# Optimization experiments

Measured on AMD Instinct MI355X. Metric: run time of the kernel, lower is better.

## Reference

```python
import jax, jax.numpy as jnp
import numpy as np

N_HEADS, D_MODEL, D_HEAD = 16, 1024, 64
BATCH, SEQ = 2, 2048
INIT_RANGE = 0.02


def setup_inputs() -> dict:
    key = jax.random.key(0)
    ks = jax.random.split(key, 5)
    x = jax.random.normal(ks[0], (BATCH, SEQ, D_MODEL), dtype=jnp.float32)
    W_Q = jax.random.normal(ks[1], (N_HEADS, D_MODEL, D_HEAD), dtype=jnp.float32) * INIT_RANGE
    W_K = jax.random.normal(ks[2], (N_HEADS, D_MODEL, D_HEAD), dtype=jnp.float32) * INIT_RANGE
    W_V = jax.random.normal(ks[3], (N_HEADS, D_MODEL, D_HEAD), dtype=jnp.float32) * INIT_RANGE
    W_O = jax.random.normal(ks[4], (N_HEADS, D_HEAD, D_MODEL), dtype=jnp.float32) * INIT_RANGE
    b_Q = jnp.zeros((N_HEADS, D_HEAD), dtype=jnp.float32)
    b_K = jnp.zeros((N_HEADS, D_HEAD), dtype=jnp.float32)
    b_V = jnp.zeros((N_HEADS, D_HEAD), dtype=jnp.float32)
    b_O = jnp.zeros((D_MODEL,), dtype=jnp.float32)
    return {"normalized_resid_pre": x, "W_Q": W_Q, "W_K": W_K, "W_V": W_V,
            "W_O": W_O, "b_Q": b_Q, "b_K": b_K, "b_V": b_V, "b_O": b_O}


def reference(normalized_resid_pre, W_Q, W_K, W_V, W_O, b_Q, b_K, b_V, b_O):
    x = normalized_resid_pre  # [b, s, d_model]
    q = jnp.einsum('bsm,hmd->bshd', x, W_Q) + b_Q  # [b, s, h, d_head]
    k = jnp.einsum('bsm,hmd->bshd', x, W_K) + b_K
    v = jnp.einsum('bsm,hmd->bshd', x, W_V) + b_V
    scores = jnp.einsum('bqhd,bkhd->bhqk', q, k) / jnp.sqrt(jnp.float32(D_HEAD))
    seq = x.shape[1]
    causal = jnp.tril(jnp.ones((seq, seq), dtype=bool))  # True where allowed
    scores = jnp.where(causal, scores, jnp.float32(-jnp.inf))
    pattern = jax.nn.softmax(scores, axis=-1)  # [b, h, q, k]
    z = jnp.einsum('bhqk,bkhd->bqhd', pattern, v)
    attn_out = jnp.einsum('bqhd,hdm->bqm', z, W_O) + b_O
    return attn_out
```

## Files before the change

kernel.cpp:

```cpp
#include <hip/hip_runtime.h>
#include <hip/hip_bf16.h>

#define BATCH 2
#define SEQL 2048
#define NH 16
#define DH 64
#define DM 1024
#define LDK 72
#define QSCALE 0.1803368801111244f
#define NTASKS 1024u

typedef __hip_bfloat16 bf16;
typedef __attribute__((ext_vector_type(8))) short  bf16x8;
typedef __attribute__((ext_vector_type(4))) float  f32x4;

__device__ __forceinline__ void gl_lds16(const void* g, void* l) {
    __builtin_amdgcn_global_load_lds(
        (const __attribute__((address_space(1))) unsigned int*)g,
        (__attribute__((address_space(3))) unsigned int*)l, 16, 0, 0);
}

__global__ __launch_bounds__(256) void xconv_kernel(
    const float* __restrict__ x, bf16* __restrict__ xb)
{
    const size_t i = ((size_t)blockIdx.x * 256 + threadIdx.x) * 4;
    const float4 v = *(const float4*)(x + i);
    bf16 o[4];
    o[0] = __float2bfloat16(v.x); o[1] = __float2bfloat16(v.y);
    o[2] = __float2bfloat16(v.z); o[3] = __float2bfloat16(v.w);
    *(uint2*)(xb + i) = *(const uint2*)o;
}

__global__ __launch_bounds__(256) void wtrans_kernel(
    const float* __restrict__ Wq, const float* __restrict__ Wk,
    const float* __restrict__ Wv, const float* __restrict__ Wo,
    bf16* __restrict__ Wt)
{
    __shared__ float ts[64][65];
    const int zi = blockIdx.z;
    const float* src = (zi == 0) ? Wq : (zi == 1) ? Wk : (zi == 2) ? Wv : Wo;
    bf16* dst = Wt + (size_t)zi * DM * DM;
    const int row0 = blockIdx.y * 64;
    const int col0 = blockIdx.x * 64;
    const int tx = threadIdx.x & 63;
    const int ty = threadIdx.x >> 6;

    if (zi < 3) {
        const int h = col0 >> 6;
        #pragma unroll
        for (int i = 0; i < 16; ++i) {
            const int r = ty + 4 * i;
            ts[r][tx] = src[h * (DM * DH) + (row0 + r) * DH + tx];
        }
    } else {
        #pragma unroll
        for (int i = 0; i < 16; ++i) {
            const int r = ty + 4 * i;
            ts[r][tx] = src[(size_t)(row0 + r) * DM + col0 + tx];
        }
    }
    __syncthreads();
    #pragma unroll
    for (int i = 0; i < 16; ++i) {
        const int rr = ty + 4 * i;
        dst[(size_t)(col0 + rr) * DM + row0 + tx] = __float2bfloat16(ts[tx][rr]);
    }
}

__global__ __launch_bounds__(256) void qkv_gemm(
    const bf16* __restrict__ xb, const bf16* __restrict__ Wt,
    const float* __restrict__ bq, const float* __restrict__ bk, const float* __restrict__ bv,
    bf16* __restrict__ qkv)
{
    __shared__ __align__(16) bf16 As[128 * 32];
    __shared__ __align__(16) bf16 Bs[128 * 32];

    const int t = threadIdx.x;
    const int lane = t & 63, w = t >> 6;
    const int ml = lane & 15, quad = lane >> 4;
    const int wr = w >> 1, wc = w & 1;
    const int bn = blockIdx.x, bm = blockIdx.y, which = blockIdx.z;

    const bf16* A0 = xb + (size_t)(bm * 128) * DM;
    const bf16* B0 = Wt + (size_t)which * DM * DM + (size_t)(bn * 128) * DM;
    const float* bias = (which == 0) ? bq : (which == 1) ? bk : bv;
    bf16* outb = qkv + (size_t)which * (BATCH * SEQL * NH * DH);
    const float oscale = (which == 0) ? QSCALE : 1.0f;

    f32x4 acc[4][4];
    #pragma unroll
    for (int i = 0; i < 4; ++i)
        #pragma unroll
        for (int j = 0; j < 4; ++j) acc[i][j] = (f32x4){0.f, 0.f, 0.f, 0.f};

    for (int kt = 0; kt < DM / 32; ++kt) {
        const int k0 = kt * 32;
        __syncthreads();
        #pragma unroll
        for (int j = 0; j < 2; ++j) {
            const int flat = t + j * 256;
            const int r = flat >> 2, c = (flat & 3) * 8;
            gl_lds16(A0 + (size_t)r * DM + k0 + c, &As[flat * 8]);
            gl_lds16(B0 + (size_t)r * DM + k0 + c, &Bs[flat * 8]);
        }
        __syncthreads();
        bf16x8 af[4], bfr[4];
        #pragma unroll
        for (int i = 0; i < 4; ++i)
            af[i] = *(const bf16x8*)&As[(wr * 64 + i * 16 + ml) * 32 + quad * 8];
        #pragma unroll
        for (int j = 0; j < 4; ++j)
            bfr[j] = *(const bf16x8*)&Bs[(wc * 64 + j * 16 + ml) * 32 + quad * 8];
        #pragma unroll
        for (int i = 0; i < 4; ++i)
            #pragma unroll
            for (int j = 0; j < 4; ++j)
                acc[i][j] = __builtin_amdgcn_mfma_f32_16x16x32_bf16(af[i], bfr[j], acc[i][j], 0, 0, 0);
    }

    float bb[4];
    #pragma unroll
    for (int j = 0; j < 4; ++j) bb[j] = bias[bn * 128 + wc * 64 + j * 16 + ml];

    if (which == 2) {
        #pragma unroll
        for (int i = 0; i < 4; ++i) {
            const int row0v = bm * 128 + wr * 64 + i * 16 + quad * 4;
            const int b = row0v >> 11;
            const int s0 = row0v & (SEQL - 1);
            #pragma unroll
            for (int j = 0; j < 4; ++j) {
                const int col = bn * 128 + wc * 64 + j * 16 + ml;
                const int h = col >> 6, d = col & 63;
                bf16 tmp[4];
                #pragma unroll
                for (int rg = 0; rg < 4; ++rg)
                    tmp[rg] = __float2bfloat16(acc[i][j][rg] + bb[j]);
                *(uint2*)&outb[(((size_t)(b * NH + h)) * DH + d) * SEQL + s0] =
                    *(const uint2*)tmp;
            }
        }
    } else {
        #pragma unroll
        for (int i = 0; i < 4; ++i) {
            #pragma unroll
            for (int rg = 0; rg < 4; ++rg) {
                const int row = bm * 128 + wr * 64 + i * 16 + quad * 4 + rg;
                const int b = row >> 11;
                const int s = row & (SEQL - 1);
                #pragma unroll
                for (int j = 0; j < 4; ++j) {
                    const int col = bn * 128 + wc * 64 + j * 16 + ml;
                    const int h = col >> 6, d = col & 63;
                    outb[(((size_t)(b * NH + h)) * SEQL + s) * DH + d] =
                        __float2bfloat16((acc[i][j][rg] + bb[j]) * oscale);
                }
            }
        }
    }
}

__global__ __launch_bounds__(256) void oproj_gemm(
    const bf16* __restrict__ zb, const bf16* __restrict__ Bt,
    const float* __restrict__ bo, float* __restrict__ out)
{
    __shared__ __align__(16) bf16 As[128 * 32];
    __shared__ __align__(16) bf16 Bs[64 * 32];

    const int t = threadIdx.x;
    const int lane = t & 63, w = t >> 6;
    const int ml = lane & 15, quad = lane >> 4;
    const int wr = w >> 1, wc = w & 1;
    const int bn = blockIdx.x, bm = blockIdx.y;

    const bf16* A0 = zb + (size_t)(bm * 128) * DM;
    const bf16* B0 = Bt + (size_t)(bn * 64) * DM;

    f32x4 acc[4][2];
    #pragma unroll
    for (int i = 0; i < 4; ++i)
        #pragma unroll
        for (int j = 0; j < 2; ++j) acc[i][j] = (f32x4){0.f, 0.f, 0.f, 0.f};

    for (int kt = 0; kt < DM / 32; ++kt) {
        const int k0 = kt * 32;
        __syncthreads();
        {
            const int r0 = t >> 2, c0 = (t & 3) * 8;
            gl_lds16(A0 + (size_t)r0 * DM + k0 + c0, &As[t * 8]);
            const int f1 = t + 256;
            const int r1 = f1 >> 2, c1 = (f1 & 3) * 8;
            gl_lds16(A0 + (size_t)r1 * DM + k0 + c1, &As[f1 * 8]);
            gl_lds16(B0 + (size_t)r0 * DM + k0 + c0, &Bs[t * 8]);
        }
        __syncthreads();
        bf16x8 af[4], bfr[2];
        #pragma unroll
        for (int i = 0; i < 4; ++i)
            af[i] = *(const bf16x8*)&As[(wr * 64 + i * 16 + ml) * 32 + quad * 8];
        #pragma unroll
        for (int j = 0; j < 2; ++j)
            bfr[j] = *(const bf16x8*)&Bs[(wc * 32 + j * 16 + ml) * 32 + quad * 8];
        #pragma unroll
        for (int i = 0; i < 4; ++i)
            #pragma unroll
            for (int j = 0; j < 2; ++j)
                acc[i][j] = __builtin_amdgcn_mfma_f32_16x16x32_bf16(af[i], bfr[j], acc[i][j], 0, 0, 0);
    }

    float bb[2];
    #pragma unroll
    for (int j = 0; j < 2; ++j) bb[j] = bo[bn * 64 + wc * 32 + j * 16 + ml];

    #pragma unroll
    for (int i = 0; i < 4; ++i) {
        #pragma unroll
        for (int rg = 0; rg < 4; ++rg) {
            const int row = bm * 128 + wr * 64 + i * 16 + quad * 4 + rg;
            #pragma unroll
            for (int j = 0; j < 2; ++j) {
                const int col = bn * 64 + wc * 32 + j * 16 + ml;
                out[(size_t)row * DM + col] = acc[i][j][rg] + bb[j];
            }
        }
    }
}

__global__ __launch_bounds__(256) void attn_kernel(
    const bf16* __restrict__ qg, const bf16* __restrict__ kg, const bf16* __restrict__ vtg,
    bf16* __restrict__ z, unsigned* __restrict__ counter)
{
    __shared__ bf16 KsS[64 * LDK];
    __shared__ bf16 VtS[64 * LDK];
    __shared__ bf16 PsS[4][16 * LDK];
    __shared__ unsigned taskS;

    const int t    = threadIdx.x;
    const int lane = t & 63;
    const int w    = t >> 6;
    const int m    = lane & 15;
    const int quad = lane >> 4;

    const int rp = t >> 3;
    const int d0 = (t & 7) * 8;

    const short ob = (m == 0) ? (short)0x3F80 : (short)0;
    const bf16x8 bones = {ob, ob, ob, ob, ob, ob, ob, ob};

    bf16* Psw = PsS[w];

    for (;;) {
        __syncthreads();
        if (t == 0) taskS = atomicAdd(counter, 1u);
        __syncthreads();
        const unsigned task = taskS;
        if (task >= NTASKS) break;

        const int qt = 31 - (int)(task >> 5);
        const int bh = (int)(task & 31u);
        const int b  = bh >> 4;
        const int h  = bh & 15;
        const int q0 = qt * 64;

        const size_t base   = (size_t)bh * SEQL * DH;
        const size_t vtbase = (size_t)bh * DH * SEQL;

        bf16x8 aq[2];
        {
            const bf16* qp = qg + base + (size_t)(q0 + w * 16 + m) * DH + quad * 8;
            aq[0] = *(const bf16x8*)(qp);
            aq[1] = *(const bf16x8*)(qp + 32);
        }

        f32x4 zacc[4];
        #pragma unroll
        for (int nt = 0; nt < 4; ++nt) zacc[nt] = (f32x4){0.f, 0.f, 0.f, 0.f};
        f32x4 lacc = (f32x4){0.f, 0.f, 0.f, 0.f};

        for (int kt = 0; kt <= qt; ++kt) {
            __syncthreads();
            {
                const bf16* kr = kg + base + (size_t)(kt * 64 + 2 * rp) * DH + d0;
                const bf16* vr = vtg + vtbase + (size_t)(2 * rp) * SEQL + kt * 64 + d0;
                const uint4 k0 = *(const uint4*)(kr);
                const uint4 k1 = *(const uint4*)(kr + DH);
                const uint4 v0 = *(const uint4*)(vr);
                const uint4 v1 = *(const uint4*)(vr + SEQL);
                *(uint4*)(&KsS[(2 * rp) * LDK + d0])     = k0;
                *(uint4*)(&KsS[(2 * rp + 1) * LDK + d0]) = k1;
                *(uint4*)(&VtS[(2 * rp) * LDK + d0])     = v0;
                *(uint4*)(&VtS[(2 * rp + 1) * LDK + d0]) = v1;
            }
            __syncthreads();

            f32x4 sc[4];
            #pragma unroll
            for (int nt = 0; nt < 4; ++nt) sc[nt] = (f32x4){0.f, 0.f, 0.f, 0.f};
            #pragma unroll
            for (int ks = 0; ks < 2; ++ks) {
                #pragma unroll
                for (int nt = 0; nt < 4; ++nt) {
                    const bf16x8 bk = *(const bf16x8*)(&KsS[(nt * 16 + m) * LDK + ks * 32 + quad * 8]);
                    sc[nt] = __builtin_amdgcn_mfma_f32_16x16x32_bf16(aq[ks], bk, sc[nt], 0, 0, 0);
                }
            }
            if (kt == qt) {
                #pragma unroll
                for (int nt = 0; nt < 4; ++nt) {
                    const int col = nt * 16 + m;
                    #pragma unroll
                    for (int rg = 0; rg < 4; ++rg) {
                        const int row = w * 16 + quad * 4 + rg;
                        if (col > row) sc[nt][rg] = -1e30f;
                    }
                }
            }

            #pragma unroll
            for (int nt = 0; nt < 4; ++nt)
                #pragma unroll
                for (int rg = 0; rg < 4; ++rg)
                    Psw[(quad * 4 + rg) * LDK + nt * 16 + m] =
                        __float2bfloat16(__builtin_exp2f(sc[nt][rg]));

            #pragma unroll
            for (int ks = 0; ks < 2; ++ks) {
                const bf16x8 ap = *(const bf16x8*)(&Psw[m * LDK + ks * 32 + quad * 8]);
                lacc = __builtin_amdgcn_mfma_f32_16x16x32_bf16(ap, bones, lacc, 0, 0, 0);
                #pragma unroll
                for (int nt = 0; nt < 4; ++nt) {
                    const bf16x8 bv = *(const bf16x8*)(&VtS[(nt * 16 + m) * LDK + ks * 32 + quad * 8]);
                    zacc[nt] = __builtin_amdgcn_mfma_f32_16x16x32_bf16(ap, bv, zacc[nt], 0, 0, 0);
                }
            }
        }

        float invl[4];
        #pragma unroll
        for (int rg = 0; rg < 4; ++rg)
            invl[rg] = 1.f / __shfl(lacc[rg], quad * 16);
        #pragma unroll
        for (int nt = 0; nt < 4; ++nt) {
            const int d = nt * 16 + m;
            #pragma unroll
            for (int rg = 0; rg < 4; ++rg) {
                const int qrow = q0 + w * 16 + quad * 4 + rg;
                z[(((size_t)b * SEQL + qrow) * NH + h) * DH + d] =
                    __float2bfloat16(zacc[nt][rg] * invl[rg]);
            }
        }
    }
}

extern "C" void kernel_launch(void* const* d_in, const int* in_sizes, int n_in,
                              void* d_out, int out_size, void* d_ws, size_t ws_size,
                              hipStream_t stream)
{
    const float* x  = (const float*)d_in[0];
    const float* Wq = (const float*)d_in[1];
    const float* Wk = (const float*)d_in[2];
    const float* Wv = (const float*)d_in[3];
    const float* Wo = (const float*)d_in[4];
    const float* bq = (const float*)d_in[5];
    const float* bk = (const float*)d_in[6];
    const float* bv = (const float*)d_in[7];
    const float* bo = (const float*)d_in[8];
    float* out = (float*)d_out;

    const size_t TOK = (size_t)BATCH * SEQL;
    const size_t QKV = TOK * DM;
    bf16* xb  = (bf16*)d_ws;
    bf16* Wt  = xb + QKV;
    bf16* qkv = Wt + 4 * (size_t)DM * DM;
    bf16* zb  = qkv + 3 * QKV;
    unsigned* counter = (unsigned*)(zb + QKV);

    hipMemsetAsync(counter, 0, sizeof(unsigned), stream);
    xconv_kernel<<<dim3(TOK * DM / 1024), 256, 0, stream>>>(x, xb);
    wtrans_kernel<<<dim3(16, 16, 4), 256, 0, stream>>>(Wq, Wk, Wv, Wo, Wt);
    qkv_gemm<<<dim3(8, 32, 3), 256, 0, stream>>>(xb, Wt, bq, bk, bv, qkv);
    attn_kernel<<<dim3(512), 256, 0, stream>>>(
        qkv, qkv + QKV, qkv + 2 * QKV, zb, counter);
    oproj_gemm<<<dim3(16, 32), 256, 0, stream>>>(zb, Wt + 3 * (size_t)DM * DM, bo, out);
}
```

Baseline: 205.5 us.

## Replace atomic persistent attention scheduler with static grid; vectorize Q/K epilogue stores

The attention kernel no longer runs as a persistent kernel that pulls tasks from an atomic counter. It now launches one block per (batch*head, query tile), with the largest query tiles given the lowest blockIdx.y, which removes the counter memset, the atomics and the per-task barriers. The QKV GEMM swaps the A and B fragment sources for the Q and K outputs so each lane holds four consecutive head dimensions, allowing packed 8-byte stores and a float4 bias load instead of scalar stores. The risk is that the static grid depends on the hardware dispatcher for load balance across uneven causal tiles.

```diff
diff --git a/kernel.cpp b/kernel.cpp
--- a/kernel.cpp
+++ b/kernel.cpp
@@ -8,7 +8,6 @@
 #define DM 1024
 #define LDK 72
 #define QSCALE 0.1803368801111244f
-#define NTASKS 1024u
 
 typedef __hip_bfloat16 bf16;
 typedef __attribute__((ext_vector_type(8))) short  bf16x8;
@@ -87,6 +86,9 @@
     bf16* outb = qkv + (size_t)which * (BATCH * SEQL * NH * DH);
     const float oscale = (which == 0) ? QSCALE : 1.0f;
 
+    const bf16* AfragSrc = (which == 2) ? As : Bs;
+    const bf16* BfragSrc = (which == 2) ? Bs : As;
+
     f32x4 acc[4][4];
     #pragma unroll
     for (int i = 0; i < 4; ++i)
@@ -107,10 +109,10 @@
         bf16x8 af[4], bfr[4];
         #pragma unroll
         for (int i = 0; i < 4; ++i)
-            af[i] = *(const bf16x8*)&As[(wr * 64 + i * 16 + ml) * 32 + quad * 8];
+            af[i] = *(const bf16x8*)&AfragSrc[(wr * 64 + i * 16 + ml) * 32 + quad * 8];
         #pragma unroll
         for (int j = 0; j < 4; ++j)
-            bfr[j] = *(const bf16x8*)&Bs[(wc * 64 + j * 16 + ml) * 32 + quad * 8];
+            bfr[j] = *(const bf16x8*)&BfragSrc[(wc * 64 + j * 16 + ml) * 32 + quad * 8];
         #pragma unroll
         for (int i = 0; i < 4; ++i)
             #pragma unroll
@@ -118,11 +120,10 @@
                 acc[i][j] = __builtin_amdgcn_mfma_f32_16x16x32_bf16(af[i], bfr[j], acc[i][j], 0, 0, 0);
     }
 
-    float bb[4];
-    #pragma unroll
-    for (int j = 0; j < 4; ++j) bb[j] = bias[bn * 128 + wc * 64 + j * 16 + ml];
-
     if (which == 2) {
+        float bb[4];
+        #pragma unroll
+        for (int j = 0; j < 4; ++j) bb[j] = bias[bn * 128 + wc * 64 + j * 16 + ml];
         #pragma unroll
         for (int i = 0; i < 4; ++i) {
             const int row0v = bm * 128 + wr * 64 + i * 16 + quad * 4;
@@ -143,18 +144,21 @@
     } else {
         #pragma unroll
         for (int i = 0; i < 4; ++i) {
-            #pragma unroll
-            for (int rg = 0; rg < 4; ++rg) {
-                const int row = bm * 128 + wr * 64 + i * 16 + quad * 4 + rg;
-                const int b = row >> 11;
-                const int s = row & (SEQL - 1);
+            const int hd0 = bn * 128 + wr * 64 + i * 16 + quad * 4;
+            const int h = hd0 >> 6, d0 = hd0 & 63;
+            const float4 bb4 = *(const float4*)&bias[hd0];
+            const float bbv[4] = {bb4.x, bb4.y, bb4.z, bb4.w};
+            #pragma unroll
+            for (int j = 0; j < 4; ++j) {
+                const int tok = bm * 128 + wc * 64 + j * 16 + ml;
+                const int b = tok >> 11;
+                const int s = tok & (SEQL - 1);
+                bf16 tmp[4];
                 #pragma unroll
-                for (int j = 0; j < 4; ++j) {
-                    const int col = bn * 128 + wc * 64 + j * 16 + ml;
-                    const int h = col >> 6, d = col & 63;
-                    outb[(((size_t)(b * NH + h)) * SEQL + s) * DH + d] =
-                        __float2bfloat16((acc[i][j][rg] + bb[j]) * oscale);
-                }
+                for (int rg = 0; rg < 4; ++rg)
+                    tmp[rg] = __float2bfloat16((acc[i][j][rg] + bbv[rg]) * oscale);
+                *(uint2*)&outb[(((size_t)(b * NH + h)) * SEQL + s) * DH + d0] =
+                    *(const uint2*)tmp;
             }
         }
     }
@@ -228,12 +232,11 @@
 
 __global__ __launch_bounds__(256) void attn_kernel(
     const bf16* __restrict__ qg, const bf16* __restrict__ kg, const bf16* __restrict__ vtg,
-    bf16* __restrict__ z, unsigned* __restrict__ counter)
+    bf16* __restrict__ z)
 {
     __shared__ bf16 KsS[64 * LDK];
     __shared__ bf16 VtS[64 * LDK];
     __shared__ bf16 PsS[4][16 * LDK];
-    __shared__ unsigned taskS;
 
     const int t    = threadIdx.x;
     const int lane = t & 63;
@@ -241,113 +244,105 @@
     const int m    = lane & 15;
     const int quad = lane >> 4;
 
+    const int bh = blockIdx.x;
+    const int b  = bh >> 4;
+    const int h  = bh & 15;
+    const int qt = (gridDim.y - 1) - blockIdx.y;
+    const int q0 = qt * 64;
+
+    const size_t base   = (size_t)bh * SEQL * DH;
+    const size_t vtbase = (size_t)bh * DH * SEQL;
+
     const int rp = t >> 3;
     const int d0 = (t & 7) * 8;
 
+    bf16x8 aq[2];
+    {
+        const bf16* qp = qg + base + (size_t)(q0 + w * 16 + m) * DH + quad * 8;
+        aq[0] = *(const bf16x8*)(qp);
+        aq[1] = *(const bf16x8*)(qp + 32);
+    }
+
     const short ob = (m == 0) ? (short)0x3F80 : (short)0;
     const bf16x8 bones = {ob, ob, ob, ob, ob, ob, ob, ob};
 
+    f32x4 zacc[4];
+    #pragma unroll
+    for (int nt = 0; nt < 4; ++nt) zacc[nt] = (f32x4){0.f, 0.f, 0.f, 0.f};
+    f32x4 lacc = (f32x4){0.f, 0.f, 0.f, 0.f};
+
     bf16* Psw = PsS[w];
 
-    for (;;) {
-        __syncthreads();
-        if (t == 0) taskS = atomicAdd(counter, 1u);
-        __syncthreads();
-        const unsigned task = taskS;
-        if (task >= NTASKS) break;
-
-        const int qt = 31 - (int)(task >> 5);
-        const int bh = (int)(task & 31u);
-        const int b  = bh >> 4;
-        const int h  = bh & 15;
-        const int q0 = qt * 64;
-
-        const size_t base   = (size_t)bh * SEQL * DH;
-        const size_t vtbase = (size_t)bh * DH * SEQL;
-
-        bf16x8 aq[2];
+    for (int kt = 0; kt <= qt; ++kt) {
+        __syncthreads();
         {
-            const bf16* qp = qg + base + (size_t)(q0 + w * 16 + m) * DH + quad * 8;
-            aq[0] = *(const bf16x8*)(qp);
-            aq[1] = *(const bf16x8*)(qp + 32);
-        }
-
-        f32x4 zacc[4];
-        #pragma unroll
-        for (int nt = 0; nt < 4; ++nt) zacc[nt] = (f32x4){0.f, 0.f, 0.f, 0.f};
-        f32x4 lacc = (f32x4){0.f, 0.f, 0.f, 0.f};
-
-        for (int kt = 0; kt <= qt; ++kt) {
-            __syncthreads();
-            {
-                const bf16* kr = kg + base + (size_t)(kt * 64 + 2 * rp) * DH + d0;
-                const bf16* vr = vtg + vtbase + (size_t)(2 * rp) * SEQL + kt * 64 + d0;
-                const uint4 k0 = *(const uint4*)(kr);
-                const uint4 k1 = *(const uint4*)(kr + DH);
-                const uint4 v0 = *(const uint4*)(vr);
-                const uint4 v1 = *(const uint4*)(vr + SEQL);
-                *(uint4*)(&KsS[(2 * rp) * LDK + d0])     = k0;
-                *(uint4*)(&KsS[(2 * rp + 1) * LDK + d0]) = k1;
-                *(uint4*)(&VtS[(2 * rp) * LDK + d0])     = v0;
-                *(uint4*)(&VtS[(2 * rp + 1) * LDK + d0]) = v1;
-            }
-            __syncthreads();
-
-            f32x4 sc[4];
-            #pragma unroll
-            for (int nt = 0; nt < 4; ++nt) sc[nt] = (f32x4){0.f, 0.f, 0.f, 0.f};
-            #pragma unroll
-            for (int ks = 0; ks < 2; ++ks) {
+            const bf16* kr = kg + base + (size_t)(kt * 64 + 2 * rp) * DH + d0;
+            const bf16* vr = vtg + vtbase + (size_t)(2 * rp) * SEQL + kt * 64 + d0;
+            const uint4 k0 = *(const uint4*)(kr);
+            const uint4 k1 = *(const uint4*)(kr + DH);
+            const uint4 v0 = *(const uint4*)(vr);
+            const uint4 v1 = *(const uint4*)(vr + SEQL);
+            *(uint4*)(&KsS[(2 * rp) * LDK + d0])     = k0;
+            *(uint4*)(&KsS[(2 * rp + 1) * LDK + d0]) = k1;
+            *(uint4*)(&VtS[(2 * rp) * LDK + d0])     = v0;
+            *(uint4*)(&VtS[(2 * rp + 1) * LDK + d0]) = v1;
+        }
+        __syncthreads();
+
+        f32x4 sc[4];
+        #pragma unroll
+        for (int nt = 0; nt < 4; ++nt) sc[nt] = (f32x4){0.f, 0.f, 0.f, 0.f};
+        #pragma unroll
+        for (int ks = 0; ks < 2; ++ks) {
+            #pragma unroll
+            for (int nt = 0; nt < 4; ++nt) {
+                const bf16x8 bk = *(const bf16x8*)(&KsS[(nt * 16 + m) * LDK + ks * 32 + quad * 8]);
+                sc[nt] = __builtin_amdgcn_mfma_f32_16x16x32_bf16(aq[ks], bk, sc[nt], 0, 0, 0);
+            }
+        }
+        if (kt == qt) {
+            #pragma unroll
+            for (int nt = 0; nt < 4; ++nt) {
+                const int col = nt * 16 + m;
                 #pragma unroll
-                for (int nt = 0; nt < 4; ++nt) {
-                    const bf16x8 bk = *(const bf16x8*)(&KsS[(nt * 16 + m) * LDK + ks * 32 + quad * 8]);
-                    sc[nt] = __builtin_amdgcn_mfma_f32_16x16x32_bf16(aq[ks], bk, sc[nt], 0, 0, 0);
+                for (int rg = 0; rg < 4; ++rg) {
+                    const int row = w * 16 + quad * 4 + rg;
+                    if (col > row) sc[nt][rg] = -1e30f;
                 }
             }
-            if (kt == qt) {
-                #pragma unroll
-                for (int nt = 0; nt < 4; ++nt) {
-                    const int col = nt * 16 + m;
-                    #pragma unroll
-                    for (int rg = 0; rg < 4; ++rg) {
-                        const int row = w * 16 + quad * 4 + rg;
-                        if (col > row) sc[nt][rg] = -1e30f;
-                    }
-                }
-            }
-
-            #pragma unroll
-            for (int nt = 0; nt < 4; ++nt)
-                #pragma unroll
-                for (int rg = 0; rg < 4; ++rg)
-                    Psw[(quad * 4 + rg) * LDK + nt * 16 + m] =
-                        __float2bfloat16(__builtin_exp2f(sc[nt][rg]));
-
-            #pragma unroll
-            for (int ks = 0; ks < 2; ++ks) {
-                const bf16x8 ap = *(const bf16x8*)(&Psw[m * LDK + ks * 32 + quad * 8]);
-                lacc = __builtin_amdgcn_mfma_f32_16x16x32_bf16(ap, bones, lacc, 0, 0, 0);
-                #pragma unroll
-                for (int nt = 0; nt < 4; ++nt) {
-                    const bf16x8 bv = *(const bf16x8*)(&VtS[(nt * 16 + m) * LDK + ks * 32 + quad * 8]);
-                    zacc[nt] = __builtin_amdgcn_mfma_f32_16x16x32_bf16(ap, bv, zacc[nt], 0, 0, 0);
-                }
-            }
-        }
-
-        float invl[4];
-        #pragma unroll
-        for (int rg = 0; rg < 4; ++rg)
-            invl[rg] = 1.f / __shfl(lacc[rg], quad * 16);
-        #pragma unroll
-        for (int nt = 0; nt < 4; ++nt) {
-            const int d = nt * 16 + m;
-            #pragma unroll
-            for (int rg = 0; rg < 4; ++rg) {
-                const int qrow = q0 + w * 16 + quad * 4 + rg;
-                z[(((size_t)b * SEQL + qrow) * NH + h) * DH + d] =
-                    __float2bfloat16(zacc[nt][rg] * invl[rg]);
-            }
+        }
+
+        #pragma unroll
+        for (int nt = 0; nt < 4; ++nt)
+            #pragma unroll
+            for (int rg = 0; rg < 4; ++rg)
+                Psw[(quad * 4 + rg) * LDK + nt * 16 + m] =
+                    __float2bfloat16(__builtin_exp2f(sc[nt][rg]));
+
+        #pragma unroll
+        for (int ks = 0; ks < 2; ++ks) {
+            const bf16x8 ap = *(const bf16x8*)(&Psw[m * LDK + ks * 32 + quad * 8]);
+            lacc = __builtin_amdgcn_mfma_f32_16x16x32_bf16(ap, bones, lacc, 0, 0, 0);
+            #pragma unroll
+            for (int nt = 0; nt < 4; ++nt) {
+                const bf16x8 bv = *(const bf16x8*)(&VtS[(nt * 16 + m) * LDK + ks * 32 + quad * 8]);
+                zacc[nt] = __builtin_amdgcn_mfma_f32_16x16x32_bf16(ap, bv, zacc[nt], 0, 0, 0);
+            }
+        }
+    }
+
+    float invl[4];
+    #pragma unroll
+    for (int rg = 0; rg < 4; ++rg)
+        invl[rg] = 1.f / __shfl(lacc[rg], quad * 16);
+    #pragma unroll
+    for (int nt = 0; nt < 4; ++nt) {
+        const int d = nt * 16 + m;
+        #pragma unroll
+        for (int rg = 0; rg < 4; ++rg) {
+            const int qrow = q0 + w * 16 + quad * 4 + rg;
+            z[(((size_t)b * SEQL + qrow) * NH + h) * DH + d] =
+                __float2bfloat16(zacc[nt][rg] * invl[rg]);
         }
     }
 }
@@ -373,13 +368,11 @@
     bf16* Wt  = xb + QKV;
     bf16* qkv = Wt + 4 * (size_t)DM * DM;
     bf16* zb  = qkv + 3 * QKV;
-    unsigned* counter = (unsigned*)(zb + QKV);
-
-    hipMemsetAsync(counter, 0, sizeof(unsigned), stream);
+
     xconv_kernel<<<dim3(TOK * DM / 1024), 256, 0, stream>>>(x, xb);
     wtrans_kernel<<<dim3(16, 16, 4), 256, 0, stream>>>(Wq, Wk, Wv, Wo, Wt);
     qkv_gemm<<<dim3(8, 32, 3), 256, 0, stream>>>(xb, Wt, bq, bk, bv, qkv);
-    attn_kernel<<<dim3(512), 256, 0, stream>>>(
-        qkv, qkv + QKV, qkv + 2 * QKV, zb, counter);
+    attn_kernel<<<dim3(BATCH * NH, SEQL / 64), 256, 0, stream>>>(
+        qkv, qkv + QKV, qkv + 2 * QKV, zb);
     oproj_gemm<<<dim3(16, 32), 256, 0, stream>>>(zb, Wt + 3 * (size_t)DM * DM, bo, out);
 }
```

After: 209.8 us. +2.1%, slower.

## Double K-step per barrier in GEMMs and use static grid for attention

Applied to the files above, without the earlier changes.

The QKV and output-projection GEMMs now load two 32-wide K slices per iteration into doubled LDS buffers. This halves the number of barrier pairs per K loop. The attention kernel drops its persistent atomic work-queue and memset and launches one block per (batch-head, query tile), with the longest tiles issued first by reversing blockIdx.y. This removes atomic and memset overhead but relies on the hardware scheduler for load balance across causal tiles of uneven length.

```diff
diff --git a/kernel.cpp b/kernel.cpp
--- a/kernel.cpp
+++ b/kernel.cpp
@@ -8,7 +8,6 @@
 #define DM 1024
 #define LDK 72
 #define QSCALE 0.1803368801111244f
-#define NTASKS 1024u
 
 typedef __hip_bfloat16 bf16;
 typedef __attribute__((ext_vector_type(8))) short  bf16x8;
@@ -72,8 +71,8 @@
     const float* __restrict__ bq, const float* __restrict__ bk, const float* __restrict__ bv,
     bf16* __restrict__ qkv)
 {
-    __shared__ __align__(16) bf16 As[128 * 32];
-    __shared__ __align__(16) bf16 Bs[128 * 32];
+    __shared__ __align__(16) bf16 As[2][128 * 32];
+    __shared__ __align__(16) bf16 Bs[2][128 * 32];
 
     const int t = threadIdx.x;
     const int lane = t & 63, w = t >> 6;
@@ -93,29 +92,37 @@
         #pragma unroll
         for (int j = 0; j < 4; ++j) acc[i][j] = (f32x4){0.f, 0.f, 0.f, 0.f};
 
-    for (int kt = 0; kt < DM / 32; ++kt) {
-        const int k0 = kt * 32;
-        __syncthreads();
-        #pragma unroll
-        for (int j = 0; j < 2; ++j) {
-            const int flat = t + j * 256;
-            const int r = flat >> 2, c = (flat & 3) * 8;
-            gl_lds16(A0 + (size_t)r * DM + k0 + c, &As[flat * 8]);
-            gl_lds16(B0 + (size_t)r * DM + k0 + c, &Bs[flat * 8]);
-        }
-        __syncthreads();
-        bf16x8 af[4], bfr[4];
-        #pragma unroll
-        for (int i = 0; i < 4; ++i)
-            af[i] = *(const bf16x8*)&As[(wr * 64 + i * 16 + ml) * 32 + quad * 8];
-        #pragma unroll
-        for (int j = 0; j < 4; ++j)
-            bfr[j] = *(const bf16x8*)&Bs[(wc * 64 + j * 16 + ml) * 32 + quad * 8];
-        #pragma unroll
-        for (int i = 0; i < 4; ++i)
+    const int r0 = t >> 2, c0 = (t & 3) * 8;
+    const int f1 = t + 256;
+    const int r1 = f1 >> 2, c1 = (f1 & 3) * 8;
+
+    for (int kt = 0; kt < DM / 64; ++kt) {
+        const int k0 = kt * 64;
+        __syncthreads();
+        #pragma unroll
+        for (int half = 0; half < 2; ++half) {
+            const int kh = k0 + half * 32;
+            gl_lds16(A0 + (size_t)r0 * DM + kh + c0, &As[half][t * 8]);
+            gl_lds16(A0 + (size_t)r1 * DM + kh + c1, &As[half][f1 * 8]);
+            gl_lds16(B0 + (size_t)r0 * DM + kh + c0, &Bs[half][t * 8]);
+            gl_lds16(B0 + (size_t)r1 * DM + kh + c1, &Bs[half][f1 * 8]);
+        }
+        __syncthreads();
+        #pragma unroll
+        for (int half = 0; half < 2; ++half) {
+            bf16x8 af[4], bfr[4];
+            #pragma unroll
+            for (int i = 0; i < 4; ++i)
+                af[i] = *(const bf16x8*)&As[half][(wr * 64 + i * 16 + ml) * 32 + quad * 8];
             #pragma unroll
             for (int j = 0; j < 4; ++j)
-                acc[i][j] = __builtin_amdgcn_mfma_f32_16x16x32_bf16(af[i], bfr[j], acc[i][j], 0, 0, 0);
+                bfr[j] = *(const bf16x8*)&Bs[half][(wc * 64 + j * 16 + ml) * 32 + quad * 8];
+            #pragma unroll
+            for (int i = 0; i < 4; ++i)
+                #pragma unroll
+                for (int j = 0; j < 4; ++j)
+                    acc[i][j] = __builtin_amdgcn_mfma_f32_16x16x32_bf16(af[i], bfr[j], acc[i][j], 0, 0, 0);
+        }
     }
 
     float bb[4];
@@ -164,8 +171,8 @@
     const bf16* __restrict__ zb, const bf16* __restrict__ Bt,
     const float* __restrict__ bo, float* __restrict__ out)
 {
-    __shared__ __align__(16) bf16 As[128 * 32];
-    __shared__ __align__(16) bf16 Bs[64 * 32];
+    __shared__ __align__(16) bf16 As[2][128 * 32];
+    __shared__ __align__(16) bf16 Bs[2][64 * 32];
 
     const int t = threadIdx.x;
     const int lane = t & 63, w = t >> 6;
@@ -182,30 +189,36 @@
         #pragma unroll
         for (int j = 0; j < 2; ++j) acc[i][j] = (f32x4){0.f, 0.f, 0.f, 0.f};
 
-    for (int kt = 0; kt < DM / 32; ++kt) {
-        const int k0 = kt * 32;
-        __syncthreads();
-        {
-            const int r0 = t >> 2, c0 = (t & 3) * 8;
-            gl_lds16(A0 + (size_t)r0 * DM + k0 + c0, &As[t * 8]);
-            const int f1 = t + 256;
-            const int r1 = f1 >> 2, c1 = (f1 & 3) * 8;
-            gl_lds16(A0 + (size_t)r1 * DM + k0 + c1, &As[f1 * 8]);
-            gl_lds16(B0 + (size_t)r0 * DM + k0 + c0, &Bs[t * 8]);
-        }
-        __syncthreads();
-        bf16x8 af[4], bfr[2];
-        #pragma unroll
-        for (int i = 0; i < 4; ++i)
-            af[i] = *(const bf16x8*)&As[(wr * 64 + i * 16 + ml) * 32 + quad * 8];
-        #pragma unroll
-        for (int j = 0; j < 2; ++j)
-            bfr[j] = *(const bf16x8*)&Bs[(wc * 32 + j * 16 + ml) * 32 + quad * 8];
-        #pragma unroll
-        for (int i = 0; i < 4; ++i)
+    const int r0 = t >> 2, c0 = (t & 3) * 8;
+    const int f1 = t + 256;
+    const int r1 = f1 >> 2, c1 = (f1 & 3) * 8;
+
+    for (int kt = 0; kt < DM / 64; ++kt) {
+        const int k0 = kt * 64;
+        __syncthreads();
+        #pragma unroll
+        for (int half = 0; half < 2; ++half) {
+            const int kh = k0 + half * 32;
+            gl_lds16(A0 + (size_t)r0 * DM + kh + c0, &As[half][t * 8]);
+            gl_lds16(A0 + (size_t)r1 * DM + kh + c1, &As[half][f1 * 8]);
+            gl_lds16(B0 + (size_t)r0 * DM + kh + c0, &Bs[half][t * 8]);
+        }
+        __syncthreads();
+        #pragma unroll
+        for (int half = 0; half < 2; ++half) {
+            bf16x8 af[4], bfr[2];
+            #pragma unroll
+            for (int i = 0; i < 4; ++i)
+                af[i] = *(const bf16x8*)&As[half][(wr * 64 + i * 16 + ml) * 32 + quad * 8];
             #pragma unroll
             for (int j = 0; j < 2; ++j)
-                acc[i][j] = __builtin_amdgcn_mfma_f32_16x16x32_bf16(af[i], bfr[j], acc[i][j], 0, 0, 0);
+                bfr[j] = *(const bf16x8*)&Bs[half][(wc * 32 + j * 16 + ml) * 32 + quad * 8];
+            #pragma unroll
+            for (int i = 0; i < 4; ++i)
+                #pragma unroll
+                for (int j = 0; j < 2; ++j)
+                    acc[i][j] = __builtin_amdgcn_mfma_f32_16x16x32_bf16(af[i], bfr[j], acc[i][j], 0, 0, 0);
+        }
     }
 
     float bb[2];
@@ -228,12 +241,11 @@
 
 __global__ __launch_bounds__(256) void attn_kernel(
     const bf16* __restrict__ qg, const bf16* __restrict__ kg, const bf16* __restrict__ vtg,
-    bf16* __restrict__ z, unsigned* __restrict__ counter)
+    bf16* __restrict__ z)
 {
     __shared__ bf16 KsS[64 * LDK];
     __shared__ bf16 VtS[64 * LDK];
     __shared__ bf16 PsS[4][16 * LDK];
-    __shared__ unsigned taskS;
 
     const int t    = threadIdx.x;
     const int lane = t & 63;
@@ -241,113 +253,105 @@
     const int m    = lane & 15;
     const int quad = lane >> 4;
 
+    const int bh = blockIdx.x;
+    const int b  = bh >> 4;
+    const int h  = bh & 15;
+    const int qt = (gridDim.y - 1) - blockIdx.y;
+    const int q0 = qt * 64;
+
+    const size_t base   = (size_t)bh * SEQL * DH;
+    const size_t vtbase = (size_t)bh * DH * SEQL;
+
     const int rp = t >> 3;
     const int d0 = (t & 7) * 8;
 
+    bf16x8 aq[2];
+    {
+        const bf16* qp = qg + base + (size_t)(q0 + w * 16 + m) * DH + quad * 8;
+        aq[0] = *(const bf16x8*)(qp);
+        aq[1] = *(const bf16x8*)(qp + 32);
+    }
+
     const short ob = (m == 0) ? (short)0x3F80 : (short)0;
     const bf16x8 bones = {ob, ob, ob, ob, ob, ob, ob, ob};
 
+    f32x4 zacc[4];
+    #pragma unroll
+    for (int nt = 0; nt < 4; ++nt) zacc[nt] = (f32x4){0.f, 0.f, 0.f, 0.f};
+    f32x4 lacc = (f32x4){0.f, 0.f, 0.f, 0.f};
+
     bf16* Psw = PsS[w];
 
-    for (;;) {
-        __syncthreads();
-        if (t == 0) taskS = atomicAdd(counter, 1u);
-        __syncthreads();
-        const unsigned task = taskS;
-        if (task >= NTASKS) break;
-
-        const int qt = 31 - (int)(task >> 5);
-        const int bh = (int)(task & 31u);
-        const int b  = bh >> 4;
-        const int h  = bh & 15;
-        const int q0 = qt * 64;
-
-        const size_t base   = (size_t)bh * SEQL * DH;
-        const size_t vtbase = (size_t)bh * DH * SEQL;
-
-        bf16x8 aq[2];
+    for (int kt = 0; kt <= qt; ++kt) {
+        __syncthreads();
         {
-            const bf16* qp = qg + base + (size_t)(q0 + w * 16 + m) * DH + quad * 8;
-            aq[0] = *(const bf16x8*)(qp);
-            aq[1] = *(const bf16x8*)(qp + 32);
-        }
-
-        f32x4 zacc[4];
-        #pragma unroll
-        for (int nt = 0; nt < 4; ++nt) zacc[nt] = (f32x4){0.f, 0.f, 0.f, 0.f};
-        f32x4 lacc = (f32x4){0.f, 0.f, 0.f, 0.f};
-
-        for (int kt = 0; kt <= qt; ++kt) {
-            __syncthreads();
-            {
-                const bf16* kr = kg + base + (size_t)(kt * 64 + 2 * rp) * DH + d0;
-                const bf16* vr = vtg + vtbase + (size_t)(2 * rp) * SEQL + kt * 64 + d0;
-                const uint4 k0 = *(const uint4*)(kr);
-                const uint4 k1 = *(const uint4*)(kr + DH);
-                const uint4 v0 = *(const uint4*)(vr);
-                const uint4 v1 = *(const uint4*)(vr + SEQL);
-                *(uint4*)(&KsS[(2 * rp) * LDK + d0])     = k0;
-                *(uint4*)(&KsS[(2 * rp + 1) * LDK + d0]) = k1;
-                *(uint4*)(&VtS[(2 * rp) * LDK + d0])     = v0;
-                *(uint4*)(&VtS[(2 * rp + 1) * LDK + d0]) = v1;
-            }
-            __syncthreads();
-
-            f32x4 sc[4];
-            #pragma unroll
-            for (int nt = 0; nt < 4; ++nt) sc[nt] = (f32x4){0.f, 0.f, 0.f, 0.f};
-            #pragma unroll
-            for (int ks = 0; ks < 2; ++ks) {
-                #pragma unroll
-                for (int nt = 0; nt < 4; ++nt) {
-                    const bf16x8 bk = *(const bf16x8*)(&KsS[(nt * 16 + m) * LDK + ks * 32 + quad * 8]);
-                    sc[nt] = __builtin_amdgcn_mfma_f32_16x16x32_bf16(aq[ks], bk, sc[nt], 0, 0, 0);
+            const bf16* kr = kg + base + (size_t)(kt * 64 + 2 * rp) * DH + d0;
+            const bf16* vr = vtg + vtbase + (size_t)(2 * rp) * SEQL + kt * 64 + d0;
+            const uint4 k0 = *(const uint4*)(kr);
+            const uint4 k1 = *(const uint4*)(kr + DH);
+            const uint4 v0 = *(const uint4*)(vr);
+            const uint4 v1 = *(const uint4*)(vr + SEQL);
+            *(uint4*)(&KsS[(2 * rp) * LDK + d0])     = k0;
+            *(uint4*)(&KsS[(2 * rp + 1) * LDK + d0]) = k1;
+            *(uint4*)(&VtS[(2 * rp) * LDK + d0])     = v0;
+            *(uint4*)(&VtS[(2 * rp + 1) * LDK + d0]) = v1;
+        }
+        __syncthreads();
+
+        f32x4 sc[4];
+        #pragma unroll
+        for (int nt = 0; nt < 4; ++nt) sc[nt] = (f32x4){0.f, 0.f, 0.f, 0.f};
+        #pragma unroll
+        for (int ks = 0; ks < 2; ++ks) {
+            #pragma unroll
+            for (int nt = 0; nt < 4; ++nt) {
+                const bf16x8 bk = *(const bf16x8*)(&KsS[(nt * 16 + m) * LDK + ks * 32 + quad * 8]);
+                sc[nt] = __builtin_amdgcn_mfma_f32_16x16x32_bf16(aq[ks], bk, sc[nt], 0, 0, 0);
+            }
+        }
+        if (kt == qt) {
+            #pragma unroll
+            for (int nt = 0; nt < 4; ++nt) {
+                const int col = nt * 16 + m;
+                #pragma unroll
+                for (int rg = 0; rg < 4; ++rg) {
+                    const int row = w * 16 + quad * 4 + rg;
+                    if (col > row) sc[nt][rg] = -1e30f;
                 }
             }
-            if (kt == qt) {
-                #pragma unroll
-                for (int nt = 0; nt < 4; ++nt) {
-                    const int col = nt * 16 + m;
-                    #pragma unroll
-                    for (int rg = 0; rg < 4; ++rg) {
-                        const int row = w * 16 + quad * 4 + rg;
-                        if (col > row) sc[nt][rg] = -1e30f;
-                    }
-                }
-            }
-
-            #pragma unroll
-            for (int nt = 0; nt < 4; ++nt)
-                #pragma unroll
-                for (int rg = 0; rg < 4; ++rg)
-                    Psw[(quad * 4 + rg) * LDK + nt * 16 + m] =
-                        __float2bfloat16(__builtin_exp2f(sc[nt][rg]));
-
-            #pragma unroll
-            for (int ks = 0; ks < 2; ++ks) {
-                const bf16x8 ap = *(const bf16x8*)(&Psw[m * LDK + ks * 32 + quad * 8]);
-                lacc = __builtin_amdgcn_mfma_f32_16x16x32_bf16(ap, bones, lacc, 0, 0, 0);
-                #pragma unroll
-                for (int nt = 0; nt < 4; ++nt) {
-                    const bf16x8 bv = *(const bf16x8*)(&VtS[(nt * 16 + m) * LDK + ks * 32 + quad * 8]);
-                    zacc[nt] = __builtin_amdgcn_mfma_f32_16x16x32_bf16(ap, bv, zacc[nt], 0, 0, 0);
-                }
-            }
-        }
-
-        float invl[4];
-        #pragma unroll
-        for (int rg = 0; rg < 4; ++rg)
-            invl[rg] = 1.f / __shfl(lacc[rg], quad * 16);
-        #pragma unroll
-        for (int nt = 0; nt < 4; ++nt) {
-            const int d = nt * 16 + m;
-            #pragma unroll
-            for (int rg = 0; rg < 4; ++rg) {
-                const int qrow = q0 + w * 16 + quad * 4 + rg;
-                z[(((size_t)b * SEQL + qrow) * NH + h) * DH + d] =
-                    __float2bfloat16(zacc[nt][rg] * invl[rg]);
-            }
+        }
+
+        #pragma unroll
+        for (int nt = 0; nt < 4; ++nt)
+            #pragma unroll
+            for (int rg = 0; rg < 4; ++rg)
+                Psw[(quad * 4 + rg) * LDK + nt * 16 + m] =
+                    __float2bfloat16(__builtin_exp2f(sc[nt][rg]));
+
+        #pragma unroll
+        for (int ks = 0; ks < 2; ++ks) {
+            const bf16x8 ap = *(const bf16x8*)(&Psw[m * LDK + ks * 32 + quad * 8]);
+            lacc = __builtin_amdgcn_mfma_f32_16x16x32_bf16(ap, bones, lacc, 0, 0, 0);
+            #pragma unroll
+            for (int nt = 0; nt < 4; ++nt) {
+                const bf16x8 bv = *(const bf16x8*)(&VtS[(nt * 16 + m) * LDK + ks * 32 + quad * 8]);
+                zacc[nt] = __builtin_amdgcn_mfma_f32_16x16x32_bf16(ap, bv, zacc[nt], 0, 0, 0);
+            }
+        }
+    }
+
+    float invl[4];
+    #pragma unroll
+    for (int rg = 0; rg < 4; ++rg)
+        invl[rg] = 1.f / __shfl(lacc[rg], quad * 16);
+    #pragma unroll
+    for (int nt = 0; nt < 4; ++nt) {
+        const int d = nt * 16 + m;
+        #pragma unroll
+        for (int rg = 0; rg < 4; ++rg) {
+            const int qrow = q0 + w * 16 + quad * 4 + rg;
+            z[(((size_t)b * SEQL + qrow) * NH + h) * DH + d] =
+                __float2bfloat16(zacc[nt][rg] * invl[rg]);
         }
     }
 }
@@ -373,13 +377,11 @@
     bf16* Wt  = xb + QKV;
     bf16* qkv = Wt + 4 * (size_t)DM * DM;
     bf16* zb  = qkv + 3 * QKV;
-    unsigned* counter = (unsigned*)(zb + QKV);
-
-    hipMemsetAsync(counter, 0, sizeof(unsigned), stream);
+
     xconv_kernel<<<dim3(TOK * DM / 1024), 256, 0, stream>>>(x, xb);
     wtrans_kernel<<<dim3(16, 16, 4), 256, 0, stream>>>(Wq, Wk, Wv, Wo, Wt);
     qkv_gemm<<<dim3(8, 32, 3), 256, 0, stream>>>(xb, Wt, bq, bk, bv, qkv);
-    attn_kernel<<<dim3(512), 256, 0, stream>>>(
-        qkv, qkv + QKV, qkv + 2 * QKV, zb, counter);
+    attn_kernel<<<dim3(BATCH * NH, SEQL / 64), 256, 0, stream>>>(
+        qkv, qkv + QKV, qkv + 2 * QKV, zb);
     oproj_gemm<<<dim3(16, 32), 256, 0, stream>>>(zb, Wt + 3 * (size_t)DM * DM, bo, out);
 }
```

New measurement: 192.0 us. 1.07x faster.
